# Optimization experiments

Hardware: AMD Instinct MI355X
Metric: run time of the kernel (lower is better)

Reference implementation:

```python
import jax, jax.numpy as jnp
import numpy as np

DIM = 96       # d_model / channels
DSTATE = 16    # SSM state size N
DINNER = 2 * DIM   # expand=2 -> 192
DTRANK = 6     # ceil(DIM/16)
K = 4          # scan directions
B, H, W = 2, 56, 56


def _ln(x, g, b, eps=1e-5):
    m = x.mean(-1, keepdims=True)
    v = x.var(-1, keepdims=True)
    return (x - m) * jax.lax.rsqrt(v + eps) * g + b


def _dwconv3(x, w, b):  # x [B,C,H,W], w [C,1,3,3] depthwise, SAME padding
    y = jax.lax.conv_general_dilated(x, w, (1, 1), [(1, 1), (1, 1)],
                                     feature_group_count=x.shape[1],
                                     dimension_numbers=('NCHW', 'OIHW', 'NCHW'))
    return y + b[None, :, None, None]


def _bn(x, g, b, m, v, eps=1e-5):  # eval-mode BatchNorm2d on NCHW
    inv = jax.lax.rsqrt(v + eps)
    return (x - m[None, :, None, None]) * (inv * g)[None, :, None, None] + b[None, :, None, None]


def _selective_scan(u, dt, A, Bs, Cs, Dp, dt_bias):
    # u, dt: [B,K,D,L]; A: [K,D,N]; Bs,Cs: [B,K,N,L]; Dp, dt_bias: [K,D]
    dt = jax.nn.softplus(dt + dt_bias[None, :, :, None])
    dA = jnp.exp(jnp.einsum('bkdl,kdn->lbkdn', dt, A))           # [L,B,K,D,N]
    dBu = jnp.einsum('bkdl,bknl,bkdl->lbkdn', dt, Bs, u)          # [L,B,K,D,N]
    Ct = jnp.moveaxis(Cs, -1, 0)                                  # [L,B,K,N]
    h0 = jnp.zeros(dA.shape[1:], dA.dtype)

    def step(h, inp):
        dA_l, dBu_l, C_l = inp
        h = dA_l * h + dBu_l
        return h, jnp.einsum('bkdn,bkn->bkd', h, C_l)

    _, ys = jax.lax.scan(step, h0, (dA, dBu, Ct))                 # ys [L,B,K,D]
    return jnp.moveaxis(ys, 0, -1) + u * Dp[None, :, :, None]     # [B,K,D,L]


def setup_inputs() -> dict:
    key = jax.random.key(0)
    ks = jax.random.split(key, 12)
    s = 0.02
    f32 = jnp.float32
    inp = {}
    inp['x'] = jax.random.normal(ks[0], (B, H, W, DIM), f32)
    # conv branch: depthwise 3x3 + BN + ReLU + 1x1 + BN
    inp['dw_w'] = jax.random.normal(ks[1], (DIM, 1, 3, 3), f32) * s
    inp['dw_b'] = jnp.zeros((DIM,), f32)
    inp['bn1_g'] = jnp.ones((DIM,), f32); inp['bn1_b'] = jnp.zeros((DIM,), f32)
    inp['bn1_m'] = jnp.zeros((DIM,), f32); inp['bn1_v'] = jnp.ones((DIM,), f32)
    inp['pw_w'] = jax.random.normal(ks[2], (DIM, DIM), f32) * s
    inp['pw_b'] = jnp.zeros((DIM,), f32)
    inp['bn2_g'] = jnp.ones((DIM,), f32); inp['bn2_b'] = jnp.zeros((DIM,), f32)
    inp['bn2_m'] = jnp.zeros((DIM,), f32); inp['bn2_v'] = jnp.ones((DIM,), f32)
    # pre-mamba LayerNorm
    inp['ln_g'] = jnp.ones((DIM,), f32); inp['ln_b'] = jnp.zeros((DIM,), f32)
    # SS2D params
    inp['in_proj_w'] = jax.random.normal(ks[3], (2 * DINNER, DIM), f32) * s
    inp['conv_w'] = jax.random.normal(ks[4], (DINNER, 1, 3, 3), f32) * s
    inp['conv_b'] = jnp.zeros((DINNER,), f32)
    inp['x_proj_w'] = jax.random.normal(ks[5], (K, DTRANK + 2 * DSTATE, DINNER), f32) * s
    inp['dt_w'] = jax.random.normal(ks[6], (K, DINNER, DTRANK), f32) * s
    inp['dt_b'] = jnp.full((K, DINNER), -4.6, f32)  # softplus(dt_b) ~= 0.01
    inp['A_logs'] = jnp.log(jnp.tile(jnp.arange(1, DSTATE + 1, dtype=f32), (K * DINNER, 1)))
    inp['Ds'] = jnp.ones((K * DINNER,), f32)
    inp['out_norm_g'] = jnp.ones((DINNER,), f32); inp['out_norm_b'] = jnp.zeros((DINNER,), f32)
    inp['out_proj_w'] = jax.random.normal(ks[7], (DIM, DINNER), f32) * s
    # fusion: Linear(2*dim, dim) + LayerNorm(dim)
    inp['fus_w'] = jax.random.normal(ks[8], (DIM, 2 * DIM), f32) * s
    inp['fus_b'] = jnp.zeros((DIM,), f32)
    inp['fus_ln_g'] = jnp.ones((DIM,), f32); inp['fus_ln_b'] = jnp.zeros((DIM,), f32)
    return inp


def reference(x, dw_w, dw_b, bn1_g, bn1_b, bn1_m, bn1_v, pw_w, pw_b,
              bn2_g, bn2_b, bn2_m, bn2_v, ln_g, ln_b,
              in_proj_w, conv_w, conv_b, x_proj_w, dt_w, dt_b, A_logs, Ds,
              out_norm_g, out_norm_b, out_proj_w, fus_w, fus_b, fus_ln_g, fus_ln_b):
    Bsz, Hh, Ww, C = x.shape
    L = Hh * Ww
    # ----- conv branch -----
    xc = jnp.transpose(x, (0, 3, 1, 2))                       # [B,C,H,W]
    c = jax.nn.relu(_bn(_dwconv3(xc, dw_w, dw_b), bn1_g, bn1_b, bn1_m, bn1_v))
    c = jnp.einsum('bchw,oc->bohw', c, pw_w) + pw_b[None, :, None, None]
    conv_out = jnp.transpose(_bn(c, bn2_g, bn2_b, bn2_m, bn2_v), (0, 2, 3, 1))
    # ----- mamba (SS2D) branch -----
    xn = _ln(x, ln_g, ln_b)
    xz = xn @ in_proj_w.T                                     # [B,H,W,2*Din]
    xm, z = jnp.split(xz, 2, axis=-1)
    xm = jnp.transpose(xm, (0, 3, 1, 2))                      # [B,Din,H,W]
    xm = jax.nn.silu(_dwconv3(xm, conv_w, conv_b))
    v1 = xm.reshape(Bsz, DINNER, L)                           # row-major scan
    v2 = jnp.transpose(xm, (0, 1, 3, 2)).reshape(Bsz, DINNER, L)  # col-major scan
    xs = jnp.stack([v1, v2, v1[..., ::-1], v2[..., ::-1]], axis=1)  # [B,4,Din,L]
    x_dbl = jnp.einsum('bkdl,kcd->bkcl', xs, x_proj_w)
    dts, Bmat, Cmat = jnp.split(x_dbl, [DTRANK, DTRANK + DSTATE], axis=2)
    dts = jnp.einsum('bkrl,kdr->bkdl', dts, dt_w)
    A = -jnp.exp(A_logs).reshape(K, DINNER, DSTATE)
    out_y = _selective_scan(xs, dts, A, Bmat, Cmat, Ds.reshape(K, DINNER), dt_b)
    y1 = out_y[:, 0]
    inv_y = out_y[:, 2:4][..., ::-1]
    y2 = inv_y[:, 0]
    y3 = jnp.transpose(inv_y[:, 1].reshape(Bsz, DINNER, Ww, Hh), (0, 1, 3, 2)).reshape(Bsz, DINNER, L)
    y4 = jnp.transpose(out_y[:, 1].reshape(Bsz, DINNER, Ww, Hh), (0, 1, 3, 2)).reshape(Bsz, DINNER, L)
    y = jnp.transpose(y1 + y2 + y3 + y4, (0, 2, 1)).reshape(Bsz, Hh, Ww, DINNER)
    y = _ln(y, out_norm_g, out_norm_b)
    y = y * jax.nn.silu(z)
    mamba_out = y @ out_proj_w.T                              # [B,H,W,C]
    # ----- fusion + residual -----
    fused = jnp.concatenate([conv_out, mamba_out], axis=-1) @ fus_w.T + fus_b
    fused = _ln(fused, fus_ln_g, fus_ln_b)
    return x + fused
```

## Files before the change

### kernel.cpp

```cpp
#include <hip/hip_runtime.h>
#include <math.h>

#define BZ 2
#define HH 56
#define WW 56
#define LL 3136
#define CC 96
#define DI 192
#define NS 16
#define RR 6
#define NT 49
#define NCH 98
#define CH 32

#define OFF_CONV   0
#define OFF_XMRAW  602112
#define OFF_Z      1806336
#define OFF_V1     3010560
#define OFF_V2     4214784
#define OFF_DT     5419008
#define OFF_BS     10235904
#define OFF_CS     10637312
#define OFF_Y      11038720
#define OFF_Y13    15855616
#define OFF_T      18264064
#define OFF_W2     19468288

__device__ __forceinline__ float softplusf(float x) {
    if (x > 20.f) return x;
    return log1pf(__expf(x));
}

__global__ __launch_bounds__(64) void k0_w2(const float* __restrict__ fus_w,
                                            const float* __restrict__ opw,
                                            float* __restrict__ W2) {
    int i = blockIdx.x * 64 + threadIdx.x;
    if (i >= CC * DI) return;
    int o = i / DI, d = i % DI;
    float acc = 0.f;
    for (int j = 0; j < CC; ++j)
        acc += fus_w[o * DI + CC + j] * opw[j * DI + d];
    W2[i] = acc;
}

__global__ __launch_bounds__(256) void k0c_negA(const float* __restrict__ A_logs,
                                                float* __restrict__ negA) {
    int i = blockIdx.x * 256 + threadIdx.x;
    if (i < 4 * DI * NS) negA[i] = -__expf(A_logs[i]);
}

__global__ __launch_bounds__(256) void k1a_dw(const float* __restrict__ x,
    const float* __restrict__ dw_w, const float* __restrict__ dw_b,
    const float* __restrict__ bn1_g, const float* __restrict__ bn1_b,
    const float* __restrict__ bn1_m, const float* __restrict__ bn1_v,
    float* __restrict__ cbuf) {
    int i = blockIdx.x * 256 + threadIdx.x;
    if (i >= BZ * LL * CC) return;
    int c = i % CC;
    int bl = i / CC;
    int l = bl % LL, b = bl / LL;
    int h = l / WW, w = l % WW;
    float acc = dw_b[c];
    #pragma unroll
    for (int dy = -1; dy <= 1; ++dy) {
        int hh = h + dy; if (hh < 0 || hh >= HH) continue;
        #pragma unroll
        for (int dx = -1; dx <= 1; ++dx) {
            int ww = w + dx; if (ww < 0 || ww >= WW) continue;
            acc += x[((b * HH + hh) * WW + ww) * CC + c] * dw_w[c * 9 + (dy + 1) * 3 + (dx + 1)];
        }
    }
    float inv = rsqrtf(bn1_v[c] + 1e-5f);
    float v = (acc - bn1_m[c]) * inv * bn1_g[c] + bn1_b[c];
    cbuf[i] = fmaxf(v, 0.f);
}

__global__ __launch_bounds__(256) void k1b_pw(const float* __restrict__ cbuf,
    const float* __restrict__ pw_w, const float* __restrict__ pw_b,
    const float* __restrict__ bn2_g, const float* __restrict__ bn2_b,
    const float* __restrict__ bn2_m, const float* __restrict__ bn2_v,
    float* __restrict__ conv_out) {
    int t0 = blockIdx.x * 64;
    int og = blockIdx.y;
    int b = blockIdx.z;
    int lane = threadIdx.x & 63;
    int wvu = __builtin_amdgcn_readfirstlane(threadIdx.x >> 6);
    __shared__ float ct[CC * 65];
    __shared__ float res[64 * 49];
    const float* cb = cbuf + (b * LL + t0) * CC;
    for (int e = threadIdx.x; e < 64 * CC; e += 256) {
        int p = e / CC, c = e % CC;
        ct[c * 65 + p] = cb[e];
    }
    __syncthreads();
    int o0 = og * 48 + wvu * 12;
    float acc[12];
    const float* pb = pw_b + o0;
    #pragma unroll
    for (int j = 0; j < 12; ++j) acc[j] = pb[j];
    const float* wb = pw_w + o0 * CC;
    for (int c = 0; c < CC; ++c) {
        float xv = ct[c * 65 + lane];
        #pragma unroll
        for (int j = 0; j < 12; ++j)
            acc[j] += xv * wb[j * CC + c];
    }
    #pragma unroll
    for (int j = 0; j < 12; ++j) {
        int o = o0 + j;
        float inv = rsqrtf(bn2_v[o] + 1e-5f);
        res[lane * 49 + wvu * 12 + j] = (acc[j] - bn2_m[o]) * inv * bn2_g[o] + bn2_b[o];
    }
    __syncthreads();
    float* ob = conv_out + (b * LL + t0) * CC + og * 48;
    for (int e = threadIdx.x; e < 64 * 48; e += 256) {
        int pl = e / 48, o = e % 48;
        ob[pl * CC + o] = res[pl * 49 + o];
    }
}

__global__ __launch_bounds__(256) void k2_inproj(const float* __restrict__ x,
    const float* __restrict__ ln_g, const float* __restrict__ ln_b,
    const float* __restrict__ ipw,
    float* __restrict__ xm_raw, float* __restrict__ z_buf) {
    int t0 = blockIdx.x * 64;
    int og = blockIdx.y;
    int b = blockIdx.z;
    int lane = threadIdx.x & 63;
    int wv = threadIdx.x >> 6;
    int wvu = __builtin_amdgcn_readfirstlane(wv);
    __shared__ float xt[64 * 97];
    __shared__ float xn[96 * 65];
    __shared__ float ps[4][64], ps2[4][64];
    const float* xb = x + (b * LL + t0) * CC;
    for (int e = threadIdx.x; e < 64 * CC; e += 256) {
        int p = e / CC, c = e % CC;
        xt[p * 97 + c] = xb[e];
    }
    __syncthreads();
    float s = 0.f, s2 = 0.f;
    #pragma unroll
    for (int j = 0; j < 24; ++j) {
        float v = xt[lane * 97 + wvu * 24 + j];
        s += v; s2 += v * v;
    }
    ps[wv][lane] = s; ps2[wv][lane] = s2;
    __syncthreads();
    float st = 0.f, st2 = 0.f;
    #pragma unroll
    for (int i = 0; i < 4; ++i) { st += ps[i][lane]; st2 += ps2[i][lane]; }
    float m = st * (1.f / 96.f);
    float inv = rsqrtf(st2 * (1.f / 96.f) - m * m + 1e-5f);
    #pragma unroll
    for (int j = 0; j < 24; ++j) {
        int c = wvu * 24 + j;
        xn[c * 65 + lane] = (xt[lane * 97 + c] - m) * inv * ln_g[c] + ln_b[c];
    }
    __syncthreads();
    float acc[12];
    #pragma unroll
    for (int j = 0; j < 12; ++j) acc[j] = 0.f;
    int o0 = og * 48 + wvu * 12;
    const float* wbase = ipw + o0 * CC;
    for (int c = 0; c < CC; ++c) {
        float xv = xn[c * 65 + lane];
        #pragma unroll
        for (int j = 0; j < 12; ++j)
            acc[j] += xv * wbase[j * CC + c];
    }
    int p = t0 + lane;
    #pragma unroll
    for (int j = 0; j < 12; ++j) {
        int out = o0 + j;
        if (out < DI) xm_raw[(b * DI + out) * LL + p] = acc[j];
        else          z_buf[(b * DI + (out - DI)) * LL + p] = acc[j];
    }
}

__global__ __launch_bounds__(256) void k3_dw(const float* __restrict__ xm_raw,
    const float* __restrict__ conv_w, const float* __restrict__ conv_b,
    float* __restrict__ v1, float* __restrict__ v2) {
    int bd = blockIdx.x;
    int half = blockIdx.y;
    int d = bd % DI;
    int h0 = half * 28;
    __shared__ float tile[28 * 57];
    const float* src = xm_raw + bd * LL;
    float wloc[9];
    #pragma unroll
    for (int i = 0; i < 9; ++i) wloc[i] = conv_w[d * 9 + i];
    float bias = conv_b[d];
    for (int e = threadIdx.x; e < 28 * WW; e += 256) {
        int hl = e / WW, w = e % WW;
        int h = h0 + hl;
        float acc = bias;
        #pragma unroll
        for (int dy = -1; dy <= 1; ++dy) {
            int hh = h + dy; if (hh < 0 || hh >= HH) continue;
            #pragma unroll
            for (int dx = -1; dx <= 1; ++dx) {
                int ww = w + dx; if (ww < 0 || ww >= WW) continue;
                acc += src[hh * WW + ww] * wloc[(dy + 1) * 3 + (dx + 1)];
            }
        }
        float sig = 1.f / (1.f + __expf(-acc));
        float v = acc * sig;
        v1[bd * LL + h * WW + w] = v;
        tile[hl * 57 + w] = v;
    }
    __syncthreads();
    for (int e = threadIdx.x; e < 28 * WW; e += 256) {
        int w = e / 28, hl = e % 28;
        v2[bd * LL + w * HH + h0 + hl] = tile[hl * 57 + w];
    }
}

__global__ __launch_bounds__(256) void k4a_xproj(const float* __restrict__ v1,
    const float* __restrict__ v2, const float* __restrict__ xpw,
    float* __restrict__ dtr_g, float* __restrict__ B_s, float* __restrict__ C_s) {
    int tile = blockIdx.x;
    int k = blockIdx.y, b = blockIdx.z;
    int lane = threadIdx.x & 63;
    int wvu = __builtin_amdgcn_readfirstlane(threadIdx.x >> 6);
    int t0 = tile * 64;
    int r0 = wvu * 10; if (r0 > 28) r0 = 28;
    const float* src = ((k & 1) == 0 ? v1 : v2) + b * DI * LL + t0;
    float acc[10];
    #pragma unroll
    for (int i = 0; i < 10; ++i) acc[i] = 0.f;
    const float* wbase = xpw + (k * 38 + r0) * DI;
    for (int d = 0; d < DI; ++d) {
        float xv = src[d * LL + lane];
        #pragma unroll
        for (int i = 0; i < 10; ++i)
            acc[i] += xv * wbase[i * DI + d];
    }
    int bk = b * 4 + k;
    int p = t0 + lane;
    #pragma unroll
    for (int i = 0; i < 10; ++i) {
        int c = r0 + i;
        if (c < RR) {
            dtr_g[(bk * RR + c) * LL + p] = acc[i];
        } else if (c < RR + NS) {
            B_s[(bk * NS + (c - RR)) * LL + p] = acc[i];
        } else {
            C_s[(bk * NS + (c - RR - NS)) * LL + p] = acc[i];
        }
    }
}

__global__ __launch_bounds__(128, 4) void k5a_scan(const float* __restrict__ dtr_g,
    const float* __restrict__ dtw, const float* __restrict__ dtb,
    const float* __restrict__ B_s, const float* __restrict__ C_s,
    const float* __restrict__ v1, const float* __restrict__ v2,
    const float* __restrict__ A_logs, float* __restrict__ y_scan,
    float* __restrict__ hl_buf, float* __restrict__ Tbuf) {
    int bx = blockIdx.x;
    int dg = bx % 3, c = bx / 3;
    int k = blockIdx.y, b = blockIdx.z;
    int bk = b * 4 + k;
    int tid = threadIdx.x;
    int lane = tid & 63;
    int wvu = __builtin_amdgcn_readfirstlane(tid >> 6);
    int d0 = dg * 64, d = d0 + lane;
    bool fwd = (k < 2);
    int s0 = fwd ? c * CH : (LL - (c + 1) * CH);
    __shared__ float dtl[64 * 32];
    __shared__ float ul[64 * 32];
    __shared__ alignas(16) float bc[32 * 32];
    const float* up  = ((k & 1) == 0 ? v1 : v2) + (b * DI + d0) * LL + s0;
    int p4 = (tid & 7) << 2;
    int row0 = tid >> 3;
    const float* dtrp = dtr_g + (bk * RR) * LL + s0 + p4;
    float4 rv0 = *(const float4*)(dtrp + 0 * LL);
    float4 rv1 = *(const float4*)(dtrp + 1 * LL);
    float4 rv2 = *(const float4*)(dtrp + 2 * LL);
    float4 rv3 = *(const float4*)(dtrp + 3 * LL);
    float4 rv4 = *(const float4*)(dtrp + 4 * LL);
    float4 rv5 = *(const float4*)(dtrp + 5 * LL);
    #pragma unroll
    for (int q = 0; q < 4; ++q) {
        int row = row0 + 16 * q;
        int dd = k * DI + d0 + row;
        const float* wr = dtw + dd * RR;
        float2 w01 = *(const float2*)(wr);
        float2 w23 = *(const float2*)(wr + 2);
        float2 w45 = *(const float2*)(wr + 4);
        float bias = dtb[dd];
        float a0 = bias, a1 = bias, a2 = bias, a3 = bias;
        a0 += rv0.x * w01.x; a1 += rv0.y * w01.x; a2 += rv0.z * w01.x; a3 += rv0.w * w01.x;
        a0 += rv1.x * w01.y; a1 += rv1.y * w01.y; a2 += rv1.z * w01.y; a3 += rv1.w * w01.y;
        a0 += rv2.x * w23.x; a1 += rv2.y * w23.x; a2 += rv2.z * w23.x; a3 += rv2.w * w23.x;
        a0 += rv3.x * w23.y; a1 += rv3.y * w23.y; a2 += rv3.z * w23.y; a3 += rv3.w * w23.y;
        a0 += rv4.x * w45.x; a1 += rv4.y * w45.x; a2 += rv4.z * w45.x; a3 += rv4.w * w45.x;
        a0 += rv5.x * w45.y; a1 += rv5.y * w45.y; a2 += rv5.z * w45.y; a3 += rv5.w * w45.y;
        float dts[4] = {softplusf(a0), softplusf(a1), softplusf(a2), softplusf(a3)};
        float4 uv = *(const float4*)(up + row * LL + p4);
        float uvv[4] = {uv.x, uv.y, uv.z, uv.w};
        int rsw = row & 31;
        #pragma unroll
        for (int t = 0; t < 4; ++t) {
            int s = fwd ? (p4 + t) : (31 - (p4 + t));
            dtl[row * 32 + (s ^ rsw)] = dts[t];
            ul [row * 32 + (s ^ rsw)] = dts[t] * uvv[t];
        }
    }
    #pragma unroll
    for (int q = 0; q < 2; ++q) {
        int e = q * 128 + tid;
        int row = e >> 3;
        int pp4 = (e & 7) << 2;
        const float* src = (row < 16 ? B_s + (bk * NS + row) * LL
                                     : C_s + (bk * NS + (row - 16)) * LL) + s0 + pp4;
        float4 v = *(const float4*)src;
        float vv[4] = {v.x, v.y, v.z, v.w};
        #pragma unroll
        for (int t = 0; t < 4; ++t) {
            int s = fwd ? (pp4 + t) : (31 - (pp4 + t));
            bc[s * 32 + (row ^ ((s & 7) << 2))] = vv[t];
        }
    }
    float Ae[8];
    const float* ap = A_logs + (k * DI + d) * NS + wvu * 8;
    #pragma unroll
    for (int n = 0; n < 8; ++n) Ae[n] = -__expf(ap[n]) * 1.442695040888963f;
    __syncthreads();
    float h[8];
    #pragma unroll
    for (int n = 0; n < 8; ++n) h[n] = 0.f;
    float cum = 0.f;
    int lbase = lane * 32;
    int lsw = lane & 31;
    int w8 = wvu * 8;
    #pragma unroll
    for (int seg = 0; seg < 4; ++seg) {
        float yv_[8];
        #pragma unroll
        for (int jj = 0; jj < 8; ++jj) {
            int j = seg * 8 + jj;
            float dtv = dtl[lbase + (j ^ lsw)];
            float du  = ul [lbase + (j ^ lsw)];
            cum += dtv;
            int cswz = (j & 7) << 2;
            const float* rb0 = &bc[j * 32 + ( w8       ^ cswz)];
            const float* rb1 = &bc[j * 32 + ((w8 +  4) ^ cswz)];
            const float* rc0 = &bc[j * 32 + ((w8 + 16) ^ cswz)];
            const float* rc1 = &bc[j * 32 + ((w8 + 20) ^ cswz)];
            float4 b0 = *(const float4*)rb0, b1 = *(const float4*)rb1;
            float4 c0 = *(const float4*)rc0, c1 = *(const float4*)rc1;
            float bv[8] = {b0.x, b0.y, b0.z, b0.w, b1.x, b1.y, b1.z, b1.w};
            float cv[8] = {c0.x, c0.y, c0.z, c0.w, c1.x, c1.y, c1.z, c1.w};
            float y = 0.f;
            #pragma unroll
            for (int n = 0; n < 8; ++n) {
                h[n] = exp2f(dtv * Ae[n]) * h[n] + du * bv[n];
                y += h[n] * cv[n];
            }
            yv_[jj] = y;
        }
        __syncthreads();
        float* dst = (wvu == 0) ? dtl : ul;
        #pragma unroll
        for (int jj = 0; jj < 8; ++jj) {
            int j = seg * 8 + jj;
            dst[lbase + (j ^ lsw)] = yv_[jj];
        }
    }
    __syncthreads();
    float* yp = y_scan + (bk * DI + d0) * LL + s0;
    #pragma unroll
    for (int q = 0; q < 4; ++q) {
        int e = q * 128 + tid;
        int row = e >> 3;
        int pp4 = (e & 7) << 2;
        int rsw = row & 31;
        float ov[4];
        #pragma unroll
        for (int t = 0; t < 4; ++t) {
            int s = fwd ? (pp4 + t) : (31 - (pp4 + t));
            ov[t] = dtl[row * 32 + (s ^ rsw)] + ul[row * 32 + (s ^ rsw)];
        }
        *(float4*)(yp + row * LL + pp4) = make_float4(ov[0], ov[1], ov[2], ov[3]);
    }
    float4* hp4 = (float4*)(hl_buf + (bk * NCH + c) * (DI * NS) + d * NS + wvu * 8);
    hp4[0] = make_float4(h[0], h[1], h[2], h[3]);
    hp4[1] = make_float4(h[4], h[5], h[6], h[7]);
    if (wvu == 0) Tbuf[(bk * NCH + c) * DI + d] = cum;
}

__global__ __launch_bounds__(64) void k5c_comb(float* __restrict__ hl_buf,
    const float* __restrict__ Tbuf, const float* __restrict__ negA) {
    int dg = blockIdx.x, k = blockIdx.y, b = blockIdx.z;
    int lane = threadIdx.x, dl = lane >> 4, n = lane & 15;
    int d = dg * 4 + dl;
    int bk = b * 4 + k;
    const int HS = DI * NS;
    float Av = negA[(k * DI + d) * NS + n];
    float* hp = hl_buf + (bk * NCH) * HS + dg * 64 + lane;
    const float* Tp = Tbuf + (bk * NCH) * DI + d;
    float hl[8], T[8];
    #pragma unroll
    for (int i = 0; i < 8; ++i) { hl[i] = hp[i * HS]; T[i] = Tp[i * DI]; }
    float H = 0.f;
    for (int cb = 0; cb < 96; cb += 8) {
        #pragma unroll
        for (int i = 0; i < 8; ++i) {
            int c = cb + i;
            float hlv = hl[i], Tv = T[i];
            int nc = c + 8;
            if (nc < NCH) { hl[i] = hp[nc * HS]; T[i] = Tp[nc * DI]; }
            hp[c * HS] = H;
            H = hlv + __expf(Av * Tv) * H;
        }
    }
    hp[96 * HS] = H;
    H = hl[0] + __expf(Av * T[0]) * H;
    hp[97 * HS] = H;
}

__global__ __launch_bounds__(256) void k5d_corr(const float* __restrict__ dtr_g,
    const float* __restrict__ dtw, const float* __restrict__ dtb,
    const float* __restrict__ C_s, const float* __restrict__ hin,
    const float* __restrict__ negA, float* __restrict__ y_scan) {
    int t = blockIdx.x;
    int k = blockIdx.y, b = blockIdx.z;
    bool fwd = (k < 2);
    int c  = fwd ? (t + 1) : (NCH - 1 - t);
    int s0 = fwd ? (t + 1) * CH : t * CH;
    int p32 = threadIdx.x & 31, sl = threadIdx.x >> 5;
    int bk = b * 4 + k;
    __shared__ float c_l[16 * 33];
    for (int e = threadIdx.x; e < 16 * CH; e += 256) {
        int n = e >> 5, s = e & 31;
        c_l[n * 33 + s] = C_s[(bk * NS + n) * LL + s0 + s];
    }
    const float* rp = dtr_g + (bk * RR) * LL + s0 + p32;
    float r[RR];
    #pragma unroll
    for (int q = 0; q < RR; ++q) r[q] = rp[q * LL];
    __syncthreads();
    for (int j = 0; j < 24; ++j) {
        int d = sl * 24 + j;
        int dd = k * DI + d;
        const float* wr = dtw + dd * RR;
        float a = dtb[dd];
        #pragma unroll
        for (int q = 0; q < RR; ++q)
            a += r[q] * wr[q];
        float dtv = softplusf(a);
        float cum = dtv;
        if (fwd) {
            #pragma unroll
            for (int off = 1; off < 32; off <<= 1) {
                float o = __shfl_up(cum, off, 32);
                if (p32 >= off) cum += o;
            }
        } else {
            #pragma unroll
            for (int off = 1; off < 32; off <<= 1) {
                float o = __shfl_down(cum, off, 32);
                if (p32 < 32 - off) cum += o;
            }
        }
        const float* hp = hin + (bk * NCH + c) * (DI * NS) + d * 16;
        const float* ap = negA + (k * DI + d) * NS;
        float acc = 0.f;
        #pragma unroll
        for (int n = 0; n < 16; ++n) {
            acc += c_l[n * 33 + p32] * __expf(ap[n] * cum) * hp[n];
        }
        y_scan[(bk * DI + d) * LL + s0 + p32] += acc;
    }
}

__global__ __launch_bounds__(256) void k5b_tr(const float* __restrict__ y_scan,
                                              float* __restrict__ y13t) {
    int idx = blockIdx.x;
    int d = idx % DI;
    int bk = idx / DI;
    int kk = bk % 2, b = bk / 2;
    int k = (kk == 0) ? 1 : 3;
    __shared__ float tile[HH * 57];
    const float* src = y_scan + ((b * 4 + k) * DI + d) * LL;
    for (int e = threadIdx.x; e < LL; e += 256) {
        int w = e / HH, h = e % HH;
        tile[h * 57 + w] = src[e];
    }
    __syncthreads();
    float* dst = y13t + idx * LL;
    for (int e = threadIdx.x; e < LL; e += 256) {
        int h = e / WW, w = e % WW;
        dst[e] = tile[h * 57 + w];
    }
}

__global__ __launch_bounds__(256) void k6_gather(const float* __restrict__ y_scan,
    const float* __restrict__ y13t, const float* __restrict__ v1,
    const float* __restrict__ z_buf, const float* __restrict__ Ds,
    const float* __restrict__ ong, const float* __restrict__ onb,
    float* __restrict__ t_buf) {
    int t0 = blockIdx.x * 16;
    int b = blockIdx.y;
    int p16 = threadIdx.x & 15, sl = threadIdx.x >> 4;
    int p = t0 + p16;
    __shared__ float yv[DI * 17];
    __shared__ float ps[16][16], ps2[16][16];
    float s = 0.f, s2 = 0.f;
    for (int j = 0; j < 12; ++j) {
        int d = sl * 12 + j;
        float dsum = Ds[d] + Ds[DI + d] + Ds[2 * DI + d] + Ds[3 * DI + d];
        float val = y_scan[((b * 4 + 0) * DI + d) * LL + p]
                  + y_scan[((b * 4 + 2) * DI + d) * LL + p]
                  + y13t[((b * 2 + 0) * DI + d) * LL + p]
                  + y13t[((b * 2 + 1) * DI + d) * LL + p]
                  + v1[(b * DI + d) * LL + p] * dsum;
        yv[d * 17 + p16] = val;
        s += val; s2 += val * val;
    }
    ps[sl][p16] = s; ps2[sl][p16] = s2;
    __syncthreads();
    float st = 0.f, st2 = 0.f;
    #pragma unroll
    for (int i = 0; i < 16; ++i) { st += ps[i][p16]; st2 += ps2[i][p16]; }
    float m = st * (1.f / 192.f);
    float inv = rsqrtf(st2 * (1.f / 192.f) - m * m + 1e-5f);
    for (int j = 0; j < 12; ++j) {
        int d = sl * 12 + j;
        float val = (yv[d * 17 + p16] - m) * inv * ong[d] + onb[d];
        float zz = z_buf[(b * DI + d) * LL + p];
        float sig = 1.f / (1.f + __expf(-zz));
        t_buf[(b * DI + d) * LL + p] = val * zz * sig;
    }
}

__global__ __launch_bounds__(256) void k7a_mm(const float* __restrict__ t_buf,
    const float* __restrict__ conv_out, const float* __restrict__ W2,
    const float* __restrict__ fus_w, const float* __restrict__ fus_b,
    float* __restrict__ fusedT) {
    int t0 = blockIdx.x * 64;
    int og = blockIdx.y;
    int b = blockIdx.z;
    int lane = threadIdx.x & 63;
    int wvu = __builtin_amdgcn_readfirstlane(threadIdx.x >> 6);
    __shared__ float ct[CC * 65];
    const float* cb = conv_out + (b * LL + t0) * CC;
    for (int e = threadIdx.x; e < 64 * CC; e += 256) {
        int p = e / CC, c = e % CC;
        ct[c * 65 + p] = cb[e];
    }
    __syncthreads();
    int o0 = og * 12 + wvu * 3;
    float acc[3];
    #pragma unroll
    for (int j = 0; j < 3; ++j) acc[j] = fus_b[o0 + j];
    int p = t0 + lane;
    const float* w2 = W2 + o0 * DI;
    for (int d = 0; d < DI; ++d) {
        float tv = t_buf[(b * DI + d) * LL + p];
        #pragma unroll
        for (int j = 0; j < 3; ++j)
            acc[j] += tv * w2[j * DI + d];
    }
    const float* fw = fus_w + o0 * DI;
    for (int c = 0; c < CC; ++c) {
        float cv = ct[c * 65 + lane];
        #pragma unroll
        for (int j = 0; j < 3; ++j)
            acc[j] += cv * fw[j * DI + c];
    }
    #pragma unroll
    for (int j = 0; j < 3; ++j)
        fusedT[(b * CC + o0 + j) * LL + p] = acc[j];
}

__global__ __launch_bounds__(256) void k7b_ln(const float* __restrict__ fusedT,
    const float* __restrict__ flg, const float* __restrict__ flb,
    const float* __restrict__ x, float* __restrict__ out) {
    int t0 = blockIdx.x * 16;
    int b = blockIdx.y;
    int p16 = threadIdx.x & 15, sl = threadIdx.x >> 4;
    __shared__ float ft[CC * 17];
    __shared__ float res[16 * 97];
    __shared__ float ps[16][16], ps2[16][16];
    for (int e = threadIdx.x; e < CC * 16; e += 256) {
        int o = e >> 4, p = e & 15;
        ft[o * 17 + p] = fusedT[(b * CC + o) * LL + t0 + p];
    }
    __syncthreads();
    float s = 0.f, s2 = 0.f;
    #pragma unroll
    for (int j = 0; j < 6; ++j) {
        float v = ft[(sl * 6 + j) * 17 + p16];
        s += v; s2 += v * v;
    }
    ps[sl][p16] = s; ps2[sl][p16] = s2;
    __syncthreads();
    float st = 0.f, st2 = 0.f;
    #pragma unroll
    for (int i = 0; i < 16; ++i) { st += ps[i][p16]; st2 += ps2[i][p16]; }
    float m = st * (1.f / 96.f);
    float inv = rsqrtf(st2 * (1.f / 96.f) - m * m + 1e-5f);
    #pragma unroll
    for (int j = 0; j < 6; ++j) {
        int o = sl * 6 + j;
        res[p16 * 97 + o] = (ft[o * 17 + p16] - m) * inv * flg[o] + flb[o];
    }
    __syncthreads();
    const float* xb = x + (b * LL + t0) * CC;
    float* ob = out + (b * LL + t0) * CC;
    for (int e = threadIdx.x; e < 16 * CC; e += 256) {
        int pl = e / CC, o = e % CC;
        ob[e] = xb[e] + res[pl * 97 + o];
    }
}

extern "C" void kernel_launch(void* const* d_in, const int* in_sizes, int n_in,
                              void* d_out, int out_size, void* d_ws, size_t ws_size,
                              hipStream_t stream) {
    const float* x        = (const float*)d_in[0];
    const float* dw_w     = (const float*)d_in[1];
    const float* dw_b     = (const float*)d_in[2];
    const float* bn1_g    = (const float*)d_in[3];
    const float* bn1_b    = (const float*)d_in[4];
    const float* bn1_m    = (const float*)d_in[5];
    const float* bn1_v    = (const float*)d_in[6];
    const float* pw_w     = (const float*)d_in[7];
    const float* pw_b     = (const float*)d_in[8];
    const float* bn2_g    = (const float*)d_in[9];
    const float* bn2_b    = (const float*)d_in[10];
    const float* bn2_m    = (const float*)d_in[11];
    const float* bn2_v    = (const float*)d_in[12];
    const float* ln_g     = (const float*)d_in[13];
    const float* ln_b     = (const float*)d_in[14];
    const float* ipw      = (const float*)d_in[15];
    const float* conv_w   = (const float*)d_in[16];
    const float* conv_b   = (const float*)d_in[17];
    const float* xpw      = (const float*)d_in[18];
    const float* dtw      = (const float*)d_in[19];
    const float* dtb      = (const float*)d_in[20];
    const float* A_logs   = (const float*)d_in[21];
    const float* Ds       = (const float*)d_in[22];
    const float* ong      = (const float*)d_in[23];
    const float* onb      = (const float*)d_in[24];
    const float* opw      = (const float*)d_in[25];
    const float* fus_w    = (const float*)d_in[26];
    const float* fus_b    = (const float*)d_in[27];
    const float* flg      = (const float*)d_in[28];
    const float* flb      = (const float*)d_in[29];

    float* ws = (float*)d_ws;
    float* conv_out = ws + OFF_CONV;
    float* xm_raw   = ws + OFF_XMRAW;
    float* z_buf    = ws + OFF_Z;
    float* v1       = ws + OFF_V1;
    float* v2       = ws + OFF_V2;
    float* B_s      = ws + OFF_BS;
    float* C_s      = ws + OFF_CS;
    float* y_scan   = ws + OFF_Y;
    float* y13t     = ws + OFF_Y13;
    float* t_buf    = ws + OFF_T;
    float* W2       = ws + OFF_W2;
    float* cbuf     = y13t;
    float* hl_buf   = y13t;
    float* Tbuf     = xm_raw;
    float* dtr_g    = xm_raw + 262144;
    float* negA     = B_s;
    float* fusedT   = y13t;
    float* out      = (float*)d_out;

    k0_w2<<<dim3((CC * DI + 63) / 64), dim3(64), 0, stream>>>(fus_w, opw, W2);
    k1a_dw<<<dim3((BZ * LL * CC + 255) / 256), dim3(256), 0, stream>>>(x, dw_w, dw_b,
                                                     bn1_g, bn1_b, bn1_m, bn1_v, cbuf);
    k1b_pw<<<dim3(NT, 2, BZ), dim3(256), 0, stream>>>(cbuf, pw_w, pw_b,
                                                   bn2_g, bn2_b, bn2_m, bn2_v, conv_out);
    k2_inproj<<<dim3(NT, 8, BZ), dim3(256), 0, stream>>>(x, ln_g, ln_b, ipw, xm_raw, z_buf);
    k3_dw<<<dim3(BZ * DI, 2), dim3(256), 0, stream>>>(xm_raw, conv_w, conv_b, v1, v2);
    k4a_xproj<<<dim3(NT, 4, BZ), dim3(256), 0, stream>>>(v1, v2, xpw, dtr_g, B_s, C_s);
    k5a_scan<<<dim3(3 * NCH, 4, BZ), dim3(128), 0, stream>>>(dtr_g, dtw, dtb, B_s, C_s,
                                                             v1, v2, A_logs,
                                                             y_scan, hl_buf, Tbuf);
    k0c_negA<<<dim3(48), dim3(256), 0, stream>>>(A_logs, negA);
    k5c_comb<<<dim3(48, 4, BZ), dim3(64), 0, stream>>>(hl_buf, Tbuf, negA);
    k5d_corr<<<dim3(NCH - 1, 4, BZ), dim3(256), 0, stream>>>(dtr_g, dtw, dtb, C_s,
                                                             hl_buf, negA, y_scan);
    k5b_tr<<<dim3(BZ * 2 * DI), dim3(256), 0, stream>>>(y_scan, y13t);
    k6_gather<<<dim3(196, BZ), dim3(256), 0, stream>>>(y_scan, y13t, v1, z_buf, Ds, ong, onb, t_buf);
    k7a_mm<<<dim3(NT, 8, BZ), dim3(256), 0, stream>>>(t_buf, conv_out, W2, fus_w, fus_b, fusedT);
    k7b_ln<<<dim3(196, BZ), dim3(256), 0, stream>>>(fusedT, flg, flb, x, out);
}
```

Measured before the change: 353.5 us.

## Precompute softplus dt in xproj and process two chunks per scan block with prefetch

The dt projection and softplus move out of the scan kernel into the x-projection kernel, which now writes a full dt tensor to the workspace. Each scan block handles two consecutive chunks and prefetches the second chunk's dt, u and B/C into registers while the first chunk is scanned. This removes redundant dt computation (repeated for each of 3 d-groups) and hides global load latency, at the cost of a large extra dt write and read to memory, higher register pressure (launch bounds lowered to 3) and half as many scan blocks.

```diff
diff --git a/kernel.cpp b/kernel.cpp
--- a/kernel.cpp
+++ b/kernel.cpp
@@ -217,7 +217,9 @@
 
 __global__ __launch_bounds__(256) void k4a_xproj(const float* __restrict__ v1,
     const float* __restrict__ v2, const float* __restrict__ xpw,
-    float* __restrict__ dtr_g, float* __restrict__ B_s, float* __restrict__ C_s) {
+    const float* __restrict__ dtw, const float* __restrict__ dtb,
+    float* __restrict__ dtr_g, float* __restrict__ B_s, float* __restrict__ C_s,
+    float* __restrict__ dt_s) {
     int tile = blockIdx.x;
     int k = blockIdx.y, b = blockIdx.z;
     int lane = threadIdx.x & 63;
@@ -237,6 +239,7 @@
     }
     int bk = b * 4 + k;
     int p = t0 + lane;
+    __shared__ float dtr_l[RR * 64];
     #pragma unroll
     for (int i = 0; i < 10; ++i) {
         int c = r0 + i;
@@ -248,16 +251,34 @@
             C_s[(bk * NS + (c - RR - NS)) * LL + p] = acc[i];
         }
     }
-}
-
-__global__ __launch_bounds__(128, 4) void k5a_scan(const float* __restrict__ dtr_g,
-    const float* __restrict__ dtw, const float* __restrict__ dtb,
+    if (wvu == 0) {
+        #pragma unroll
+        for (int i = 0; i < RR; ++i) dtr_l[i * 64 + lane] = acc[i];
+    }
+    __syncthreads();
+    float r[RR];
+    #pragma unroll
+    for (int q = 0; q < RR; ++q) r[q] = dtr_l[q * 64 + lane];
+    float* dst = dt_s + bk * DI * LL + p;
+    for (int i = 0; i < 48; ++i) {
+        int dloc = wvu * 48 + i;
+        int dd = k * DI + dloc;
+        const float* wr = dtw + dd * RR;
+        float a = dtb[dd];
+        #pragma unroll
+        for (int q = 0; q < RR; ++q)
+            a += r[q] * wr[q];
+        dst[dloc * LL] = softplusf(a);
+    }
+}
+
+__global__ __launch_bounds__(128, 3) void k5a_scan(const float* __restrict__ dt_s,
     const float* __restrict__ B_s, const float* __restrict__ C_s,
     const float* __restrict__ v1, const float* __restrict__ v2,
     const float* __restrict__ A_logs, float* __restrict__ y_scan,
     float* __restrict__ hl_buf, float* __restrict__ Tbuf) {
     int bx = blockIdx.x;
-    int dg = bx % 3, c = bx / 3;
+    int dg = bx % 3, cp = bx / 3;
     int k = blockIdx.y, b = blockIdx.z;
     int bk = b * 4 + k;
     int tid = threadIdx.x;
@@ -265,128 +286,225 @@
     int wvu = __builtin_amdgcn_readfirstlane(tid >> 6);
     int d0 = dg * 64, d = d0 + lane;
     bool fwd = (k < 2);
-    int s0 = fwd ? c * CH : (LL - (c + 1) * CH);
+    int cA = 2 * cp, cB = 2 * cp + 1;
+    int s0A = fwd ? cA * CH : (LL - (cA + 1) * CH);
+    int s0B = fwd ? cB * CH : (LL - (cB + 1) * CH);
     __shared__ float dtl[64 * 32];
     __shared__ float ul[64 * 32];
     __shared__ alignas(16) float bc[32 * 32];
-    const float* up  = ((k & 1) == 0 ? v1 : v2) + (b * DI + d0) * LL + s0;
     int p4 = (tid & 7) << 2;
     int row0 = tid >> 3;
-    const float* dtrp = dtr_g + (bk * RR) * LL + s0 + p4;
-    float4 rv0 = *(const float4*)(dtrp + 0 * LL);
-    float4 rv1 = *(const float4*)(dtrp + 1 * LL);
-    float4 rv2 = *(const float4*)(dtrp + 2 * LL);
-    float4 rv3 = *(const float4*)(dtrp + 3 * LL);
-    float4 rv4 = *(const float4*)(dtrp + 4 * LL);
-    float4 rv5 = *(const float4*)(dtrp + 5 * LL);
+    const float* dtp = dt_s + (bk * DI + d0) * LL;
+    const float* up  = ((k & 1) == 0 ? v1 : v2) + (b * DI + d0) * LL;
+
+    float4 Ad[4], Au[4], Abc[2];
     #pragma unroll
     for (int q = 0; q < 4; ++q) {
         int row = row0 + 16 * q;
-        int dd = k * DI + d0 + row;
-        const float* wr = dtw + dd * RR;
-        float2 w01 = *(const float2*)(wr);
-        float2 w23 = *(const float2*)(wr + 2);
-        float2 w45 = *(const float2*)(wr + 4);
-        float bias = dtb[dd];
-        float a0 = bias, a1 = bias, a2 = bias, a3 = bias;
-        a0 += rv0.x * w01.x; a1 += rv0.y * w01.x; a2 += rv0.z * w01.x; a3 += rv0.w * w01.x;
-        a0 += rv1.x * w01.y; a1 += rv1.y * w01.y; a2 += rv1.z * w01.y; a3 += rv1.w * w01.y;
-        a0 += rv2.x * w23.x; a1 += rv2.y * w23.x; a2 += rv2.z * w23.x; a3 += rv2.w * w23.x;
-        a0 += rv3.x * w23.y; a1 += rv3.y * w23.y; a2 += rv3.z * w23.y; a3 += rv3.w * w23.y;
-        a0 += rv4.x * w45.x; a1 += rv4.y * w45.x; a2 += rv4.z * w45.x; a3 += rv4.w * w45.x;
-        a0 += rv5.x * w45.y; a1 += rv5.y * w45.y; a2 += rv5.z * w45.y; a3 += rv5.w * w45.y;
-        float dts[4] = {softplusf(a0), softplusf(a1), softplusf(a2), softplusf(a3)};
-        float4 uv = *(const float4*)(up + row * LL + p4);
-        float uvv[4] = {uv.x, uv.y, uv.z, uv.w};
+        Ad[q] = *(const float4*)(dtp + row * LL + s0A + p4);
+        Au[q] = *(const float4*)(up  + row * LL + s0A + p4);
+    }
+    #pragma unroll
+    for (int q = 0; q < 2; ++q) {
+        int e = q * 128 + tid;
+        int brow = e >> 3, bp4 = (e & 7) << 2;
+        const float* src = (brow < 16 ? B_s + (bk * NS + brow) * LL
+                                      : C_s + (bk * NS + (brow - 16)) * LL) + s0A + bp4;
+        Abc[q] = *(const float4*)src;
+    }
+    float Ae[8];
+    {
+        const float* ap = A_logs + (k * DI + d) * NS + wvu * 8;
+        #pragma unroll
+        for (int n = 0; n < 8; ++n) Ae[n] = -__expf(ap[n]) * 1.442695040888963f;
+    }
+    #pragma unroll
+    for (int q = 0; q < 4; ++q) {
+        int row = row0 + 16 * q;
         int rsw = row & 31;
+        float dv[4] = {Ad[q].x, Ad[q].y, Ad[q].z, Ad[q].w};
+        float uv[4] = {Au[q].x, Au[q].y, Au[q].z, Au[q].w};
         #pragma unroll
         for (int t = 0; t < 4; ++t) {
             int s = fwd ? (p4 + t) : (31 - (p4 + t));
-            dtl[row * 32 + (s ^ rsw)] = dts[t];
-            ul [row * 32 + (s ^ rsw)] = dts[t] * uvv[t];
+            dtl[row * 32 + (s ^ rsw)] = dv[t];
+            ul [row * 32 + (s ^ rsw)] = dv[t] * uv[t];
         }
     }
     #pragma unroll
     for (int q = 0; q < 2; ++q) {
         int e = q * 128 + tid;
-        int row = e >> 3;
-        int pp4 = (e & 7) << 2;
-        const float* src = (row < 16 ? B_s + (bk * NS + row) * LL
-                                     : C_s + (bk * NS + (row - 16)) * LL) + s0 + pp4;
-        float4 v = *(const float4*)src;
-        float vv[4] = {v.x, v.y, v.z, v.w};
+        int brow = e >> 3, bp4 = (e & 7) << 2;
+        float vv[4] = {Abc[q].x, Abc[q].y, Abc[q].z, Abc[q].w};
         #pragma unroll
         for (int t = 0; t < 4; ++t) {
-            int s = fwd ? (pp4 + t) : (31 - (pp4 + t));
-            bc[s * 32 + (row ^ ((s & 7) << 2))] = vv[t];
-        }
-    }
-    float Ae[8];
-    const float* ap = A_logs + (k * DI + d) * NS + wvu * 8;
-    #pragma unroll
-    for (int n = 0; n < 8; ++n) Ae[n] = -__expf(ap[n]) * 1.442695040888963f;
-    __syncthreads();
-    float h[8];
-    #pragma unroll
-    for (int n = 0; n < 8; ++n) h[n] = 0.f;
-    float cum = 0.f;
+            int s = fwd ? (bp4 + t) : (31 - (bp4 + t));
+            bc[s * 32 + (brow ^ ((s & 7) << 2))] = vv[t];
+        }
+    }
+    __syncthreads();
+    float4 Bd[4], Bu[4], Bbc[2];
+    #pragma unroll
+    for (int q = 0; q < 4; ++q) {
+        int row = row0 + 16 * q;
+        Bd[q] = *(const float4*)(dtp + row * LL + s0B + p4);
+        Bu[q] = *(const float4*)(up  + row * LL + s0B + p4);
+    }
+    #pragma unroll
+    for (int q = 0; q < 2; ++q) {
+        int e = q * 128 + tid;
+        int brow = e >> 3, bp4 = (e & 7) << 2;
+        const float* src = (brow < 16 ? B_s + (bk * NS + brow) * LL
+                                      : C_s + (bk * NS + (brow - 16)) * LL) + s0B + bp4;
+        Bbc[q] = *(const float4*)src;
+    }
     int lbase = lane * 32;
     int lsw = lane & 31;
     int w8 = wvu * 8;
-    #pragma unroll
-    for (int seg = 0; seg < 4; ++seg) {
-        float yv_[8];
-        #pragma unroll
-        for (int jj = 0; jj < 8; ++jj) {
-            int j = seg * 8 + jj;
-            float dtv = dtl[lbase + (j ^ lsw)];
-            float du  = ul [lbase + (j ^ lsw)];
-            cum += dtv;
-            int cswz = (j & 7) << 2;
-            const float* rb0 = &bc[j * 32 + ( w8       ^ cswz)];
-            const float* rb1 = &bc[j * 32 + ((w8 +  4) ^ cswz)];
-            const float* rc0 = &bc[j * 32 + ((w8 + 16) ^ cswz)];
-            const float* rc1 = &bc[j * 32 + ((w8 + 20) ^ cswz)];
-            float4 b0 = *(const float4*)rb0, b1 = *(const float4*)rb1;
-            float4 c0 = *(const float4*)rc0, c1 = *(const float4*)rc1;
-            float bv[8] = {b0.x, b0.y, b0.z, b0.w, b1.x, b1.y, b1.z, b1.w};
-            float cv[8] = {c0.x, c0.y, c0.z, c0.w, c1.x, c1.y, c1.z, c1.w};
-            float y = 0.f;
+    {
+        float h[8];
+        #pragma unroll
+        for (int n = 0; n < 8; ++n) h[n] = 0.f;
+        float cum = 0.f;
+        #pragma unroll
+        for (int seg = 0; seg < 4; ++seg) {
+            float yv_[8];
             #pragma unroll
-            for (int n = 0; n < 8; ++n) {
-                h[n] = exp2f(dtv * Ae[n]) * h[n] + du * bv[n];
-                y += h[n] * cv[n];
+            for (int jj = 0; jj < 8; ++jj) {
+                int j = seg * 8 + jj;
+                float dtv = dtl[lbase + (j ^ lsw)];
+                float du  = ul [lbase + (j ^ lsw)];
+                cum += dtv;
+                int cswz = (j & 7) << 2;
+                const float* rb0 = &bc[j * 32 + ( w8       ^ cswz)];
+                const float* rb1 = &bc[j * 32 + ((w8 +  4) ^ cswz)];
+                const float* rc0 = &bc[j * 32 + ((w8 + 16) ^ cswz)];
+                const float* rc1 = &bc[j * 32 + ((w8 + 20) ^ cswz)];
+                float4 b0 = *(const float4*)rb0, b1 = *(const float4*)rb1;
+                float4 c0 = *(const float4*)rc0, c1 = *(const float4*)rc1;
+                float bv[8] = {b0.x, b0.y, b0.z, b0.w, b1.x, b1.y, b1.z, b1.w};
+                float cv[8] = {c0.x, c0.y, c0.z, c0.w, c1.x, c1.y, c1.z, c1.w};
+                float y = 0.f;
+                #pragma unroll
+                for (int n = 0; n < 8; ++n) {
+                    h[n] = exp2f(dtv * Ae[n]) * h[n] + du * bv[n];
+                    y += h[n] * cv[n];
+                }
+                yv_[jj] = y;
             }
-            yv_[jj] = y;
+            __syncthreads();
+            float* dst = (wvu == 0) ? dtl : ul;
+            #pragma unroll
+            for (int jj = 0; jj < 8; ++jj) {
+                int j = seg * 8 + jj;
+                dst[lbase + (j ^ lsw)] = yv_[jj];
+            }
         }
         __syncthreads();
-        float* dst = (wvu == 0) ? dtl : ul;
-        #pragma unroll
-        for (int jj = 0; jj < 8; ++jj) {
-            int j = seg * 8 + jj;
-            dst[lbase + (j ^ lsw)] = yv_[jj];
-        }
-    }
-    __syncthreads();
-    float* yp = y_scan + (bk * DI + d0) * LL + s0;
+        float* yp = y_scan + (bk * DI + d0) * LL + s0A;
+        #pragma unroll
+        for (int q = 0; q < 4; ++q) {
+            int e = q * 128 + tid;
+            int row = e >> 3, pp4 = (e & 7) << 2;
+            int rsw = row & 31;
+            float ov[4];
+            #pragma unroll
+            for (int t = 0; t < 4; ++t) {
+                int s = fwd ? (pp4 + t) : (31 - (pp4 + t));
+                ov[t] = dtl[row * 32 + (s ^ rsw)] + ul[row * 32 + (s ^ rsw)];
+            }
+            *(float4*)(yp + row * LL + pp4) = make_float4(ov[0], ov[1], ov[2], ov[3]);
+        }
+        float4* hp4 = (float4*)(hl_buf + (bk * NCH + cA) * (DI * NS) + d * NS + wvu * 8);
+        hp4[0] = make_float4(h[0], h[1], h[2], h[3]);
+        hp4[1] = make_float4(h[4], h[5], h[6], h[7]);
+        if (wvu == 0) Tbuf[(bk * NCH + cA) * DI + d] = cum;
+    }
+    __syncthreads();
     #pragma unroll
     for (int q = 0; q < 4; ++q) {
+        int row = row0 + 16 * q;
+        int rsw = row & 31;
+        float dv[4] = {Bd[q].x, Bd[q].y, Bd[q].z, Bd[q].w};
+        float uv[4] = {Bu[q].x, Bu[q].y, Bu[q].z, Bu[q].w};
+        #pragma unroll
+        for (int t = 0; t < 4; ++t) {
+            int s = fwd ? (p4 + t) : (31 - (p4 + t));
+            dtl[row * 32 + (s ^ rsw)] = dv[t];
+            ul [row * 32 + (s ^ rsw)] = dv[t] * uv[t];
+        }
+    }
+    #pragma unroll
+    for (int q = 0; q < 2; ++q) {
         int e = q * 128 + tid;
-        int row = e >> 3;
-        int pp4 = (e & 7) << 2;
-        int rsw = row & 31;
-        float ov[4];
+        int brow = e >> 3, bp4 = (e & 7) << 2;
+        float vv[4] = {Bbc[q].x, Bbc[q].y, Bbc[q].z, Bbc[q].w};
         #pragma unroll
         for (int t = 0; t < 4; ++t) {
-            int s = fwd ? (pp4 + t) : (31 - (pp4 + t));
-            ov[t] = dtl[row * 32 + (s ^ rsw)] + ul[row * 32 + (s ^ rsw)];
-        }
-        *(float4*)(yp + row * LL + pp4) = make_float4(ov[0], ov[1], ov[2], ov[3]);
-    }
-    float4* hp4 = (float4*)(hl_buf + (bk * NCH + c) * (DI * NS) + d * NS + wvu * 8);
-    hp4[0] = make_float4(h[0], h[1], h[2], h[3]);
-    hp4[1] = make_float4(h[4], h[5], h[6], h[7]);
-    if (wvu == 0) Tbuf[(bk * NCH + c) * DI + d] = cum;
+            int s = fwd ? (bp4 + t) : (31 - (bp4 + t));
+            bc[s * 32 + (brow ^ ((s & 7) << 2))] = vv[t];
+        }
+    }
+    __syncthreads();
+    {
+        float h[8];
+        #pragma unroll
+        for (int n = 0; n < 8; ++n) h[n] = 0.f;
+        float cum = 0.f;
+        #pragma unroll
+        for (int seg = 0; seg < 4; ++seg) {
+            float yv_[8];
+            #pragma unroll
+            for (int jj = 0; jj < 8; ++jj) {
+                int j = seg * 8 + jj;
+                float dtv = dtl[lbase + (j ^ lsw)];
+                float du  = ul [lbase + (j ^ lsw)];
+                cum += dtv;
+                int cswz = (j & 7) << 2;
+                const float* rb0 = &bc[j * 32 + ( w8       ^ cswz)];
+                const float* rb1 = &bc[j * 32 + ((w8 +  4) ^ cswz)];
+                const float* rc0 = &bc[j * 32 + ((w8 + 16) ^ cswz)];
+                const float* rc1 = &bc[j * 32 + ((w8 + 20) ^ cswz)];
+                float4 b0 = *(const float4*)rb0, b1 = *(const float4*)rb1;
+                float4 c0 = *(const float4*)rc0, c1 = *(const float4*)rc1;
+                float bv[8] = {b0.x, b0.y, b0.z, b0.w, b1.x, b1.y, b1.z, b1.w};
+                float cv[8] = {c0.x, c0.y, c0.z, c0.w, c1.x, c1.y, c1.z, c1.w};
+                float y = 0.f;
+                #pragma unroll
+                for (int n = 0; n < 8; ++n) {
+                    h[n] = exp2f(dtv * Ae[n]) * h[n] + du * bv[n];
+                    y += h[n] * cv[n];
+                }
+                yv_[jj] = y;
+            }
+            __syncthreads();
+            float* dst = (wvu == 0) ? dtl : ul;
+            #pragma unroll
+            for (int jj = 0; jj < 8; ++jj) {
+                int j = seg * 8 + jj;
+                dst[lbase + (j ^ lsw)] = yv_[jj];
+            }
+        }
+        __syncthreads();
+        float* yp = y_scan + (bk * DI + d0) * LL + s0B;
+        #pragma unroll
+        for (int q = 0; q < 4; ++q) {
+            int e = q * 128 + tid;
+            int row = e >> 3, pp4 = (e & 7) << 2;
+            int rsw = row & 31;
+            float ov[4];
+            #pragma unroll
+            for (int t = 0; t < 4; ++t) {
+                int s = fwd ? (pp4 + t) : (31 - (pp4 + t));
+                ov[t] = dtl[row * 32 + (s ^ rsw)] + ul[row * 32 + (s ^ rsw)];
+            }
+            *(float4*)(yp + row * LL + pp4) = make_float4(ov[0], ov[1], ov[2], ov[3]);
+        }
+        float4* hp4 = (float4*)(hl_buf + (bk * NCH + cB) * (DI * NS) + d * NS + wvu * 8);
+        hp4[0] = make_float4(h[0], h[1], h[2], h[3]);
+        hp4[1] = make_float4(h[4], h[5], h[6], h[7]);
+        if (wvu == 0) Tbuf[(bk * NCH + cB) * DI + d] = cum;
+    }
 }
 
 __global__ __launch_bounds__(64) void k5c_comb(float* __restrict__ hl_buf,
@@ -655,6 +773,7 @@
     float* z_buf    = ws + OFF_Z;
     float* v1       = ws + OFF_V1;
     float* v2       = ws + OFF_V2;
+    float* dt_s     = ws + OFF_DT;
     float* B_s      = ws + OFF_BS;
     float* C_s      = ws + OFF_CS;
     float* y_scan   = ws + OFF_Y;
@@ -676,8 +795,9 @@
                                                    bn2_g, bn2_b, bn2_m, bn2_v, conv_out);
     k2_inproj<<<dim3(NT, 8, BZ), dim3(256), 0, stream>>>(x, ln_g, ln_b, ipw, xm_raw, z_buf);
     k3_dw<<<dim3(BZ * DI, 2), dim3(256), 0, stream>>>(xm_raw, conv_w, conv_b, v1, v2);
-    k4a_xproj<<<dim3(NT, 4, BZ), dim3(256), 0, stream>>>(v1, v2, xpw, dtr_g, B_s, C_s);
-    k5a_scan<<<dim3(3 * NCH, 4, BZ), dim3(128), 0, stream>>>(dtr_g, dtw, dtb, B_s, C_s,
+    k4a_xproj<<<dim3(NT, 4, BZ), dim3(256), 0, stream>>>(v1, v2, xpw, dtw, dtb,
+                                                         dtr_g, B_s, C_s, dt_s);
+    k5a_scan<<<dim3(3 * (NCH / 2), 4, BZ), dim3(128), 0, stream>>>(dt_s, B_s, C_s,
                                                              v1, v2, A_logs,
                                                              y_scan, hl_buf, Tbuf);
     k0c_negA<<<dim3(48), dim3(256), 0, stream>>>(A_logs, negA);
```

Result: slower. 383.0 us (+8.3%).
